# Kernel tuning notes

Hardware: AMD Instinct MI355X
Metric: run time of the kernel (lower is better)

## Reference

```python
import jax, jax.numpy as jnp
import numpy as np

B, T, D, H = 4, 2048, 1024, 16
HD = D // H  # head dim = 64


def setup_inputs() -> dict:
    key = jax.random.key(0)
    ks = jax.random.split(key, 9)
    s_in = 1.0 / np.sqrt(D)
    return {
        "token_embedding": jax.random.normal(ks[0], (B, T, D), dtype=jnp.float32),
        # per-head projections, batched over head axis: [H, D, HD]
        "Wq": jax.random.normal(ks[1], (H, D, HD), dtype=jnp.float32) * s_in,
        "bq": jnp.zeros((H, HD), dtype=jnp.float32),
        "Wk": jax.random.normal(ks[2], (H, D, HD), dtype=jnp.float32) * s_in,
        "bk": jnp.zeros((H, HD), dtype=jnp.float32),
        "Wv": jax.random.normal(ks[3], (H, D, HD), dtype=jnp.float32) * s_in,
        "bv": jnp.zeros((H, HD), dtype=jnp.float32),
        "Wo": jax.random.normal(ks[4], (D, D), dtype=jnp.float32) * s_in,
        "bo": jnp.zeros((D,), dtype=jnp.float32),
    }


def _mha(x, Wq, bq, Wk, bk, Wv, bv, Wo, bo):
    # x: [B,T,D]; per-head proj -> [B,H,T,HD]
    q = jnp.einsum('btd,hde->bhte', x, Wq) + bq[None, :, None, :]
    k = jnp.einsum('btd,hde->bhte', x, Wk) + bk[None, :, None, :]
    v = jnp.einsum('btd,hde->bhte', x, Wv) + bv[None, :, None, :]
    scores = jnp.einsum('bhte,bhse->bhts', q, k) / jnp.sqrt(jnp.float32(HD))
    causal = jnp.tril(jnp.ones((T, T), dtype=bool))
    scores = jnp.where(causal[None, None], scores, jnp.float32(-jnp.inf))
    attn = jax.nn.softmax(scores, axis=-1)
    ctx = jnp.einsum('bhts,bhse->bhte', attn, v)  # [B,H,T,HD]
    # concat heads (head order matches ModuleList order) -> [B,T,D]
    cat = jnp.transpose(ctx, (0, 2, 1, 3)).reshape(B, T, D)
    return cat @ Wo + bo


def reference(token_embedding, Wq, bq, Wk, bk, Wv, bv, Wo, bo):
    return _mha(token_embedding, Wq, bq, Wk, bk, Wv, bv, Wo, bo)
```

## Files before the change

### kernel.cpp

```cpp
#include <hip/hip_runtime.h>
#include <hip/hip_bf16.h>
#include <stdint.h>
#include <stddef.h>

#define B_ 4
#define T_ 2048
#define D_ 1024
#define H_ 16
#define HD_ 64
#define LDQKV (3 * D_)

typedef __attribute__((ext_vector_type(8))) __bf16 bf16x8;
typedef __attribute__((ext_vector_type(4))) float f32x4;
typedef __attribute__((ext_vector_type(16))) float f32x16;

#define AS1V const __attribute__((address_space(1))) void*
#define AS3V __attribute__((address_space(3))) void*

__device__ inline float cross32_max(float x) { return fmaxf(x, __shfl_xor(x, 32)); }
__device__ inline float cross32_sum(float x) { return x + __shfl_xor(x, 32); }

__global__ void cvt_x_kernel(const float* __restrict__ x, __bf16* __restrict__ xb, int n8) {
    int stride = gridDim.x * blockDim.x;
    for (int i = blockIdx.x * blockDim.x + threadIdx.x; i < n8; i += stride) {
        const float4* p = (const float4*)(x + (size_t)i * 8);
        float4 a = p[0], b = p[1];
        bf16x8 o;
        o[0] = (__bf16)a.x; o[1] = (__bf16)a.y; o[2] = (__bf16)a.z; o[3] = (__bf16)a.w;
        o[4] = (__bf16)b.x; o[5] = (__bf16)b.y; o[6] = (__bf16)b.z; o[7] = (__bf16)b.w;
        *(bf16x8*)(xb + (size_t)i * 8) = o;
    }
}

__global__ void build_wT_kernel(const float* __restrict__ Wq, const float* __restrict__ Wk,
                                const float* __restrict__ Wv, __bf16* __restrict__ wT) {
    int which = blockIdx.x, h = blockIdx.y, d0 = blockIdx.z * 4;
    const float* W = (which == 0) ? Wq : (which == 1) ? Wk : Wv;
    int e = threadIdx.x & 63, dd = threadIdx.x >> 6;
    float v = W[((size_t)h * D_ + d0 + dd) * HD_ + e];
    wT[((size_t)which * D_ + h * HD_ + e) * D_ + d0 + dd] = (__bf16)v;
}

__global__ void build_woT_kernel(const float* __restrict__ Wo, __bf16* __restrict__ woT) {
    int k = blockIdx.x;
    for (int n = threadIdx.x; n < D_; n += blockDim.x)
        woT[(size_t)n * D_ + k] = (__bf16)Wo[(size_t)k * D_ + n];
}

__global__ void build_bias_kernel(const float* __restrict__ bq, const float* __restrict__ bk,
                                  const float* __restrict__ bv, float* __restrict__ bqkv) {
    int n = blockIdx.x * blockDim.x + threadIdx.x;
    if (n >= 3 * D_) return;
    const float* b = (n < D_) ? bq : (n < 2 * D_) ? bk : bv;
    bqkv[n] = b[n & (D_ - 1)];
}

template <typename OutT>
__global__ __launch_bounds__(256, 3)
void gemm_bt_kernel(const __bf16* __restrict__ A, const __bf16* __restrict__ Bt,
                    OutT* __restrict__ C, const float* __restrict__ bias,
                    int M, int N, int K, int lda, int ldb, int ldc) {
    __shared__ __bf16 lsA[128 * 64];
    __shared__ __bf16 lsB[128 * 64];
    const int tid = threadIdx.x;
    const int lane = tid & 63;
    const int wave = tid >> 6;
    const int wr = wave >> 1, wc = wave & 1;
    const int lc = lane & 15, lg = lane >> 4;
    const long row0 = (long)blockIdx.y * 128;
    const long col0 = (long)blockIdx.x * 128;

    f32x4 acc[4][4];
#pragma unroll
    for (int mi = 0; mi < 4; mi++)
#pragma unroll
        for (int ni = 0; ni < 4; ni++)
#pragma unroll
            for (int q = 0; q < 4; q++) acc[mi][ni][q] = 0.f;

    const int s_row = tid >> 3, s_k8 = tid & 7;

    for (int k0 = 0; k0 < K; k0 += 64) {
        __syncthreads();
#pragma unroll
        for (int c2 = 0; c2 < 4; c2++) {
            const __bf16* ga = A + (row0 + c2 * 32 + s_row) * (long)lda + k0 + s_k8 * 8;
            const __bf16* gb = Bt + (col0 + c2 * 32 + s_row) * (long)ldb + k0 + s_k8 * 8;
            __bf16* la = lsA + ((c2 << 8) + (wave << 6)) * 8;
            __bf16* lb = lsB + ((c2 << 8) + (wave << 6)) * 8;
            __builtin_amdgcn_global_load_lds((AS1V)ga, (AS3V)la, 16, 0, 0);
            __builtin_amdgcn_global_load_lds((AS1V)gb, (AS3V)lb, 16, 0, 0);
        }
        __syncthreads();
#pragma unroll
        for (int kk = 0; kk < 2; kk++) {
            bf16x8 af[4], bf_[4];
#pragma unroll
            for (int mi = 0; mi < 4; mi++)
                af[mi] = *(const bf16x8*)(lsA + (wr * 64 + mi * 16 + lc) * 64 + (kk * 4 + lg) * 8);
#pragma unroll
            for (int ni = 0; ni < 4; ni++)
                bf_[ni] = *(const bf16x8*)(lsB + (wc * 64 + ni * 16 + lc) * 64 + (kk * 4 + lg) * 8);
#pragma unroll
            for (int mi = 0; mi < 4; mi++)
#pragma unroll
                for (int ni = 0; ni < 4; ni++)
                    acc[mi][ni] =
                        __builtin_amdgcn_mfma_f32_16x16x32_bf16(af[mi], bf_[ni], acc[mi][ni], 0, 0, 0);
        }
    }

#pragma unroll
    for (int mi = 0; mi < 4; mi++) {
#pragma unroll
        for (int ni = 0; ni < 4; ni++) {
            long r0 = row0 + wr * 64 + mi * 16 + lg * 4;
            long cc = col0 + wc * 64 + ni * 16 + lc;
            float bv = bias[cc];
#pragma unroll
            for (int q = 0; q < 4; q++) {
                float v = acc[mi][ni][q] + bv;
                C[(r0 + q) * (long)ldc + cc] = (OutT)v;
            }
        }
    }
}

__global__ void transpose_v_kernel(const __bf16* __restrict__ qkv, __bf16* __restrict__ vT) {
    __shared__ __bf16 tile[64][72];
    const int bh = blockIdx.y, t0 = blockIdx.x * 64;
    const int b = bh >> 4, h = bh & 15;
    const int r = threadIdx.x >> 2, c16 = (threadIdx.x & 3) * 16;
    const __bf16* src = qkv + (size_t)(b * T_ + t0 + r) * LDQKV + 2 * D_ + h * HD_ + c16;
    *(bf16x8*)&tile[r][c16] = *(const bf16x8*)src;
    *(bf16x8*)&tile[r][c16 + 8] = *(const bf16x8*)(src + 8);
    __syncthreads();
    bf16x8 v0, v1;
#pragma unroll
    for (int j = 0; j < 8; j++) v0[j] = tile[c16 + j][r];
#pragma unroll
    for (int j = 0; j < 8; j++) v1[j] = tile[c16 + 8 + j][r];
    __bf16* dst = vT + (size_t)(bh * HD_ + r) * T_ + t0 + c16;
    *(bf16x8*)dst = v0;
    *(bf16x8*)(dst + 8) = v1;
}

__global__ __launch_bounds__(256, 4)
void attn_kernel(const __bf16* __restrict__ qkv, const __bf16* __restrict__ vT,
                 __bf16* __restrict__ ctx) {
    __shared__ __bf16 lsK[64 * 64];
    __shared__ __bf16 lsV[64 * 64];
    const int tid = threadIdx.x;
    const int lane = tid & 63, w = tid >> 6;
    const int l31 = lane & 31, hi = lane >> 5;
    const int bid = blockIdx.x;
    const int xcd = bid & 7, idx = bid >> 3;
    const int bh = xcd * 8 + (idx & 7);
    const int slot = idx >> 3;
    const int chunk = (int)((0x742065138ADC9BEFULL >> (slot * 4)) & 15ULL);
    const int b = bh >> 4, h = bh & 15;
    const float K2 = 0.125f * 1.44269504f;

    const __bf16* kbase = qkv + (size_t)(b * T_) * LDQKV + D_ + h * HD_;
    const __bf16* vbase = vT + (size_t)bh * HD_ * T_;

    int s_row[2], s_ch[2];
#pragma unroll
    for (int c2 = 0; c2 < 2; c2++) {
        int idx2 = c2 * 256 + tid;
        s_row[c2] = idx2 >> 3;
        s_ch[c2] = idx2 & 7;
    }

    const int q0 = chunk * 128;
    const int qw = q0 + w * 32;
    const int myq = qw + l31;

    const __bf16* qbase = qkv + (size_t)(b * T_ + myq) * LDQKV + h * HD_;
    bf16x8 qf[4];
#pragma unroll
    for (int kf = 0; kf < 4; kf++) qf[kf] = *(const bf16x8*)(qbase + kf * 16 + hi * 8);

    f32x16 accO[2];
#pragma unroll
    for (int eo = 0; eo < 2; eo++)
#pragma unroll
        for (int r = 0; r < 16; r++) accO[eo][r] = 0.f;
    float m_r = -1e30f, l_r = 0.f;

    bf16x8 rK[2], rV[2];
    auto loadKV = [&](int kv0) {
#pragma unroll
        for (int c2 = 0; c2 < 2; c2++) {
            rK[c2] = *(const bf16x8*)(kbase + (size_t)(kv0 + s_row[c2]) * LDQKV + s_ch[c2] * 8);
            rV[c2] = *(const bf16x8*)(vbase + (size_t)s_row[c2] * T_ + kv0 + s_ch[c2] * 8);
        }
    };

    const int ntiles = 2 * (chunk + 1);
    loadKV(0);
    for (int it = 0; it < ntiles; ++it) {
        const int kv0 = it << 6;
        __syncthreads();
#pragma unroll
        for (int c2 = 0; c2 < 2; c2++) {
            *(bf16x8*)(lsK + s_row[c2] * 64 + ((s_ch[c2] ^ (s_row[c2] & 7)) << 3)) = rK[c2];
            *(bf16x8*)(lsV + s_row[c2] * 64 + ((s_ch[c2] ^ (s_row[c2] & 7)) << 3)) = rV[c2];
        }
        __syncthreads();
        if (it + 1 < ntiles) loadKV((it + 1) << 6);

        if (kv0 > qw + 31) continue;

        f32x16 st[2];
        __builtin_amdgcn_s_setprio(1);
#pragma unroll
        for (int kh = 0; kh < 2; kh++) {
            f32x16 a;
#pragma unroll
            for (int r = 0; r < 16; r++) a[r] = 0.f;
#pragma unroll
            for (int kf = 0; kf < 4; kf++) {
                int row = kh * 32 + l31;
                int ch = (kf << 1) | hi;
                bf16x8 kfrag = *(const bf16x8*)(lsK + row * 64 + ((ch ^ (row & 7)) << 3));
                a = __builtin_amdgcn_mfma_f32_32x32x16_bf16(kfrag, qf[kf], a, 0, 0, 0);
            }
            st[kh] = a;
        }
        __builtin_amdgcn_s_setprio(0);

        if (kv0 + 63 > qw) {
            const int qmk = myq - kv0 - 4 * hi;
#pragma unroll
            for (int kh = 0; kh < 2; kh++)
#pragma unroll
                for (int r = 0; r < 16; r++) {
                    int kvl = (r & 3) + 8 * (r >> 2) + kh * 32;
                    if (kvl > qmk) st[kh][r] = -1e30f;
                }
        }

        float red[16];
#pragma unroll
        for (int r = 0; r < 16; r++) red[r] = fmaxf(st[0][r], st[1][r]);
#pragma unroll
        for (int s2 = 8; s2 >= 1; s2 >>= 1)
#pragma unroll
            for (int r = 0; r < s2; r++) red[r] = fmaxf(red[r], red[r + s2]);
        float pmax = cross32_max(red[0]);

        if (!__all(pmax - m_r <= 64.f)) {
            float m_new = fmaxf(m_r, pmax);
            float alpha = exp2f((m_r - m_new) * K2);
            l_r *= alpha;
#pragma unroll
            for (int eo = 0; eo < 2; eo++)
#pragma unroll
                for (int r = 0; r < 16; r++) accO[eo][r] *= alpha;
            m_r = m_new;
        }

        const float mb = m_r * K2;
#pragma unroll
        for (int kh = 0; kh < 2; kh++)
#pragma unroll
            for (int r = 0; r < 16; r++) st[kh][r] = exp2f(fmaf(st[kh][r], K2, -mb));

        float sr[16];
#pragma unroll
        for (int r = 0; r < 16; r++) sr[r] = st[0][r] + st[1][r];
#pragma unroll
        for (int s2 = 8; s2 >= 1; s2 >>= 1)
#pragma unroll
            for (int r = 0; r < s2; r++) sr[r] += sr[r + s2];
        l_r += cross32_sum(sr[0]);

        union BW { unsigned u[4]; bf16x8 v; };
        bf16x8 pfrag[4];
        auto pack2 = [](float a, float b) -> unsigned {
            union { __bf16 h[2]; unsigned u; } x;
            x.h[0] = (__bf16)a;
            x.h[1] = (__bf16)b;
            return x.u;
        };
#pragma unroll
        for (int kh = 0; kh < 2; kh++)
#pragma unroll
            for (int sub = 0; sub < 2; sub++) {
                int base = sub * 8;
                unsigned W1 = pack2(st[kh][base + 0], st[kh][base + 1]);
                unsigned W3 = pack2(st[kh][base + 2], st[kh][base + 3]);
                unsigned W2 = pack2(st[kh][base + 4], st[kh][base + 5]);
                unsigned W4 = pack2(st[kh][base + 6], st[kh][base + 7]);
                unsigned X1 = (unsigned)__shfl_xor((int)W1, 32);
                unsigned X2 = (unsigned)__shfl_xor((int)W2, 32);
                unsigned X3 = (unsigned)__shfl_xor((int)W3, 32);
                unsigned X4 = (unsigned)__shfl_xor((int)W4, 32);
                BW bw;
                bw.u[0] = hi ? X2 : W1;
                bw.u[1] = hi ? X4 : W3;
                bw.u[2] = hi ? W2 : X1;
                bw.u[3] = hi ? W4 : X3;
                pfrag[kh * 2 + sub] = bw.v;
            }

        __builtin_amdgcn_s_setprio(1);
#pragma unroll
        for (int eo = 0; eo < 2; eo++) {
#pragma unroll
            for (int ks = 0; ks < 4; ks++) {
                int row = eo * 32 + l31;
                int ch = (ks << 1) | hi;
                bf16x8 vfrag = *(const bf16x8*)(lsV + row * 64 + ((ch ^ (row & 7)) << 3));
                accO[eo] = __builtin_amdgcn_mfma_f32_32x32x16_bf16(vfrag, pfrag[ks], accO[eo], 0, 0, 0);
            }
        }
        __builtin_amdgcn_s_setprio(0);
    }

    float invl = 1.0f / l_r;
    __bf16* cb = ctx + (size_t)(b * T_ + myq) * D_ + h * HD_;
#pragma unroll
    for (int eo = 0; eo < 2; eo++)
#pragma unroll
        for (int r = 0; r < 16; r++) {
            int e = eo * 32 + (r & 3) + 8 * (r >> 2) + 4 * hi;
            cb[e] = (__bf16)(accO[eo][r] * invl);
        }
}

extern "C" void kernel_launch(void* const* d_in, const int* in_sizes, int n_in,
                              void* d_out, int out_size, void* d_ws, size_t ws_size,
                              hipStream_t stream) {
    const float* x = (const float*)d_in[0];
    const float* Wq = (const float*)d_in[1];
    const float* bq = (const float*)d_in[2];
    const float* Wk = (const float*)d_in[3];
    const float* bk = (const float*)d_in[4];
    const float* Wv = (const float*)d_in[5];
    const float* bv = (const float*)d_in[6];
    const float* Wo = (const float*)d_in[7];
    const float* bo = (const float*)d_in[8];
    float* out = (float*)d_out;

    char* ws = (char*)d_ws;
    size_t off = 0;
    auto alloc = [&](size_t bytes) -> void* {
        off = (off + 255) & ~(size_t)255;
        void* p = ws + off;
        off += bytes;
        return p;
    };
    __bf16* xb = (__bf16*)alloc((size_t)B_ * T_ * D_ * 2);
    __bf16* wT = (__bf16*)alloc((size_t)3 * D_ * D_ * 2);
    float* bqkv = (float*)alloc((size_t)3 * D_ * 4);
    __bf16* woT = (__bf16*)alloc((size_t)D_ * D_ * 2);
    __bf16* qkv = (__bf16*)alloc((size_t)B_ * T_ * 3 * D_ * 2);
    __bf16* vTb = (__bf16*)alloc((size_t)B_ * H_ * HD_ * T_ * 2);
    __bf16* ctx = (__bf16*)alloc((size_t)B_ * T_ * D_ * 2);
    (void)ws_size;
    (void)in_sizes;
    (void)n_in;
    (void)out_size;

    cvt_x_kernel<<<2048, 256, 0, stream>>>(x, xb, B_ * T_ * D_ / 8);
    build_wT_kernel<<<dim3(3, H_, D_ / 4), 256, 0, stream>>>(Wq, Wk, Wv, wT);
    build_woT_kernel<<<D_, 256, 0, stream>>>(Wo, woT);
    build_bias_kernel<<<12, 256, 0, stream>>>(bq, bk, bv, bqkv);

    gemm_bt_kernel<__bf16><<<dim3(3 * D_ / 128, B_ * T_ / 128), 256, 0, stream>>>(
        xb, wT, qkv, bqkv, B_ * T_, 3 * D_, D_, D_, D_, 3 * D_);

    transpose_v_kernel<<<dim3(T_ / 64, B_ * H_), 256, 0, stream>>>(qkv, vTb);

    attn_kernel<<<1024, 256, 0, stream>>>(qkv, vTb, ctx);

    gemm_bt_kernel<float><<<dim3(D_ / 128, B_ * T_ / 128), 256, 0, stream>>>(
        ctx, woT, out, bo, B_ * T_, D_, D_, D_, D_, D_);
}
```

Before: 228.8 us.

## Double-buffer 128-wide KV tiles in LDS for causal attention kernel

The attention kernel now stages 128-row K/V tiles into double-buffered LDS. This drops to one barrier per tile and lets the next tile's global loads run while the current tile is computed in two 64-wide sub-steps. The block-to-chunk mapping is replaced by a simple descending/ascending order, and the GEMM launch-bounds occupancy hint is raised from 3 to 4. LDS use grows fourfold, so attention occupancy drops (launch bounds lowered to 2) and register pressure rises from the extra prefetch registers.

```diff
diff --git a/kernel.cpp b/kernel.cpp
--- a/kernel.cpp
+++ b/kernel.cpp
@@ -56,7 +56,7 @@
 }
 
 template <typename OutT>
-__global__ __launch_bounds__(256, 3)
+__global__ __launch_bounds__(256, 4)
 void gemm_bt_kernel(const __bf16* __restrict__ A, const __bf16* __restrict__ Bt,
                     OutT* __restrict__ C, const float* __restrict__ bias,
                     int M, int N, int K, int lda, int ldb, int ldc) {
@@ -145,11 +145,11 @@
     *(bf16x8*)(dst + 8) = v1;
 }
 
-__global__ __launch_bounds__(256, 4)
+__global__ __launch_bounds__(256, 2)
 void attn_kernel(const __bf16* __restrict__ qkv, const __bf16* __restrict__ vT,
                  __bf16* __restrict__ ctx) {
-    __shared__ __bf16 lsK[64 * 64];
-    __shared__ __bf16 lsV[64 * 64];
+    __shared__ __bf16 lsK[2][128 * 64];
+    __shared__ __bf16 lsV[2][64 * 128];
     const int tid = threadIdx.x;
     const int lane = tid & 63, w = tid >> 6;
     const int l31 = lane & 31, hi = lane >> 5;
@@ -157,19 +157,19 @@
     const int xcd = bid & 7, idx = bid >> 3;
     const int bh = xcd * 8 + (idx & 7);
     const int slot = idx >> 3;
-    const int chunk = (int)((0x742065138ADC9BEFULL >> (slot * 4)) & 15ULL);
+    const int chunk = (slot < 8) ? (15 - slot) : (slot - 8);
     const int b = bh >> 4, h = bh & 15;
     const float K2 = 0.125f * 1.44269504f;
 
     const __bf16* kbase = qkv + (size_t)(b * T_) * LDQKV + D_ + h * HD_;
     const __bf16* vbase = vT + (size_t)bh * HD_ * T_;
 
-    int s_row[2], s_ch[2];
-#pragma unroll
-    for (int c2 = 0; c2 < 2; c2++) {
-        int idx2 = c2 * 256 + tid;
-        s_row[c2] = idx2 >> 3;
-        s_ch[c2] = idx2 & 7;
+    int krow[4], kch[4], vrow[4], vch[4];
+#pragma unroll
+    for (int c = 0; c < 4; c++) {
+        int i2 = c * 256 + tid;
+        krow[c] = i2 >> 3;  kch[c] = i2 & 7;
+        vrow[c] = i2 >> 4;  vch[c] = i2 & 15;
     }
 
     const int q0 = chunk * 128;
@@ -188,135 +188,152 @@
         for (int r = 0; r < 16; r++) accO[eo][r] = 0.f;
     float m_r = -1e30f, l_r = 0.f;
 
-    bf16x8 rK[2], rV[2];
+    bf16x8 rK[4], rV[4];
     auto loadKV = [&](int kv0) {
 #pragma unroll
-        for (int c2 = 0; c2 < 2; c2++) {
-            rK[c2] = *(const bf16x8*)(kbase + (size_t)(kv0 + s_row[c2]) * LDQKV + s_ch[c2] * 8);
-            rV[c2] = *(const bf16x8*)(vbase + (size_t)s_row[c2] * T_ + kv0 + s_ch[c2] * 8);
+        for (int c = 0; c < 4; c++) {
+            rK[c] = *(const bf16x8*)(kbase + (size_t)(kv0 + krow[c]) * LDQKV + kch[c] * 8);
+            rV[c] = *(const bf16x8*)(vbase + (size_t)vrow[c] * T_ + kv0 + vch[c] * 8);
         }
     };
-
-    const int ntiles = 2 * (chunk + 1);
+    auto writeLDS = [&](int bi) {
+#pragma unroll
+        for (int c = 0; c < 4; c++) {
+            *(bf16x8*)(&lsK[bi][0] + krow[c] * 64 + ((kch[c] ^ (krow[c] & 7)) << 3)) = rK[c];
+            *(bf16x8*)(&lsV[bi][0] + vrow[c] * 128 + ((vch[c] ^ (vrow[c] & 15)) << 3)) = rV[c];
+        }
+    };
+
+    const int ntiles = chunk + 1;
     loadKV(0);
+    writeLDS(0);
+    if (ntiles > 1) loadKV(128);
+    __syncthreads();
+    int cur = 0;
+
     for (int it = 0; it < ntiles; ++it) {
-        const int kv0 = it << 6;
-        __syncthreads();
-#pragma unroll
-        for (int c2 = 0; c2 < 2; c2++) {
-            *(bf16x8*)(lsK + s_row[c2] * 64 + ((s_ch[c2] ^ (s_row[c2] & 7)) << 3)) = rK[c2];
-            *(bf16x8*)(lsV + s_row[c2] * 64 + ((s_ch[c2] ^ (s_row[c2] & 7)) << 3)) = rV[c2];
-        }
-        __syncthreads();
-        if (it + 1 < ntiles) loadKV((it + 1) << 6);
-
-        if (kv0 > qw + 31) continue;
-
-        f32x16 st[2];
-        __builtin_amdgcn_s_setprio(1);
-#pragma unroll
-        for (int kh = 0; kh < 2; kh++) {
-            f32x16 a;
-#pragma unroll
-            for (int r = 0; r < 16; r++) a[r] = 0.f;
-#pragma unroll
-            for (int kf = 0; kf < 4; kf++) {
-                int row = kh * 32 + l31;
-                int ch = (kf << 1) | hi;
-                bf16x8 kfrag = *(const bf16x8*)(lsK + row * 64 + ((ch ^ (row & 7)) << 3));
-                a = __builtin_amdgcn_mfma_f32_32x32x16_bf16(kfrag, qf[kf], a, 0, 0, 0);
-            }
-            st[kh] = a;
-        }
-        __builtin_amdgcn_s_setprio(0);
-
-        if (kv0 + 63 > qw) {
-            const int qmk = myq - kv0 - 4 * hi;
+        const int kv0 = it << 7;
+        const __bf16* lk = &lsK[cur][0];
+        const __bf16* lv = &lsV[cur][0];
+
+#pragma unroll
+        for (int sub = 0; sub < 2; ++sub) {
+            const int kv0s = kv0 + sub * 64;
+            if (kv0s > qw + 31) break;
+
+            f32x16 st[2];
+            __builtin_amdgcn_s_setprio(1);
+#pragma unroll
+            for (int kh = 0; kh < 2; kh++) {
+                f32x16 a;
+#pragma unroll
+                for (int r = 0; r < 16; r++) a[r] = 0.f;
+#pragma unroll
+                for (int kf = 0; kf < 4; kf++) {
+                    int row = sub * 64 + kh * 32 + l31;
+                    int ch = (kf << 1) | hi;
+                    bf16x8 kfrag = *(const bf16x8*)(lk + row * 64 + ((ch ^ (row & 7)) << 3));
+                    a = __builtin_amdgcn_mfma_f32_32x32x16_bf16(kfrag, qf[kf], a, 0, 0, 0);
+                }
+                st[kh] = a;
+            }
+            __builtin_amdgcn_s_setprio(0);
+
+            if (kv0s + 63 > qw) {
+                const int qmk = myq - kv0s - 4 * hi;
+#pragma unroll
+                for (int kh = 0; kh < 2; kh++)
+#pragma unroll
+                    for (int r = 0; r < 16; r++) {
+                        int kvl = (r & 3) + 8 * (r >> 2) + kh * 32;
+                        if (kvl > qmk) st[kh][r] = -1e30f;
+                    }
+            }
+
+            float red[16];
+#pragma unroll
+            for (int r = 0; r < 16; r++) red[r] = fmaxf(st[0][r], st[1][r]);
+#pragma unroll
+            for (int s2 = 8; s2 >= 1; s2 >>= 1)
+#pragma unroll
+                for (int r = 0; r < s2; r++) red[r] = fmaxf(red[r], red[r + s2]);
+            float pmax = cross32_max(red[0]);
+
+            if (!__all(pmax - m_r <= 64.f)) {
+                float m_new = fmaxf(m_r, pmax);
+                float alpha = exp2f((m_r - m_new) * K2);
+                l_r *= alpha;
+#pragma unroll
+                for (int eo = 0; eo < 2; eo++)
+#pragma unroll
+                    for (int r = 0; r < 16; r++) accO[eo][r] *= alpha;
+                m_r = m_new;
+            }
+
+            const float mb = m_r * K2;
 #pragma unroll
             for (int kh = 0; kh < 2; kh++)
 #pragma unroll
-                for (int r = 0; r < 16; r++) {
-                    int kvl = (r & 3) + 8 * (r >> 2) + kh * 32;
-                    if (kvl > qmk) st[kh][r] = -1e30f;
+                for (int r = 0; r < 16; r++) st[kh][r] = exp2f(fmaf(st[kh][r], K2, -mb));
+
+            float sr[16];
+#pragma unroll
+            for (int r = 0; r < 16; r++) sr[r] = st[0][r] + st[1][r];
+#pragma unroll
+            for (int s2 = 8; s2 >= 1; s2 >>= 1)
+#pragma unroll
+                for (int r = 0; r < s2; r++) sr[r] += sr[r + s2];
+            l_r += cross32_sum(sr[0]);
+
+            union BW { unsigned u[4]; bf16x8 v; };
+            bf16x8 pfrag[4];
+            auto pack2 = [](float a, float b) -> unsigned {
+                union { __bf16 h[2]; unsigned u; } x;
+                x.h[0] = (__bf16)a;
+                x.h[1] = (__bf16)b;
+                return x.u;
+            };
+#pragma unroll
+            for (int kh = 0; kh < 2; kh++)
+#pragma unroll
+                for (int sb = 0; sb < 2; sb++) {
+                    int base = sb * 8;
+                    unsigned W1 = pack2(st[kh][base + 0], st[kh][base + 1]);
+                    unsigned W3 = pack2(st[kh][base + 2], st[kh][base + 3]);
+                    unsigned W2 = pack2(st[kh][base + 4], st[kh][base + 5]);
+                    unsigned W4 = pack2(st[kh][base + 6], st[kh][base + 7]);
+                    unsigned X1 = (unsigned)__shfl_xor((int)W1, 32);
+                    unsigned X2 = (unsigned)__shfl_xor((int)W2, 32);
+                    unsigned X3 = (unsigned)__shfl_xor((int)W3, 32);
+                    unsigned X4 = (unsigned)__shfl_xor((int)W4, 32);
+                    BW bw;
+                    bw.u[0] = hi ? X2 : W1;
+                    bw.u[1] = hi ? X4 : W3;
+                    bw.u[2] = hi ? W2 : X1;
+                    bw.u[3] = hi ? W4 : X3;
+                    pfrag[kh * 2 + sb] = bw.v;
                 }
-        }
-
-        float red[16];
-#pragma unroll
-        for (int r = 0; r < 16; r++) red[r] = fmaxf(st[0][r], st[1][r]);
-#pragma unroll
-        for (int s2 = 8; s2 >= 1; s2 >>= 1)
-#pragma unroll
-            for (int r = 0; r < s2; r++) red[r] = fmaxf(red[r], red[r + s2]);
-        float pmax = cross32_max(red[0]);
-
-        if (!__all(pmax - m_r <= 64.f)) {
-            float m_new = fmaxf(m_r, pmax);
-            float alpha = exp2f((m_r - m_new) * K2);
-            l_r *= alpha;
-#pragma unroll
-            for (int eo = 0; eo < 2; eo++)
-#pragma unroll
-                for (int r = 0; r < 16; r++) accO[eo][r] *= alpha;
-            m_r = m_new;
-        }
-
-        const float mb = m_r * K2;
-#pragma unroll
-        for (int kh = 0; kh < 2; kh++)
-#pragma unroll
-            for (int r = 0; r < 16; r++) st[kh][r] = exp2f(fmaf(st[kh][r], K2, -mb));
-
-        float sr[16];
-#pragma unroll
-        for (int r = 0; r < 16; r++) sr[r] = st[0][r] + st[1][r];
-#pragma unroll
-        for (int s2 = 8; s2 >= 1; s2 >>= 1)
-#pragma unroll
-            for (int r = 0; r < s2; r++) sr[r] += sr[r + s2];
-        l_r += cross32_sum(sr[0]);
-
-        union BW { unsigned u[4]; bf16x8 v; };
-        bf16x8 pfrag[4];
-        auto pack2 = [](float a, float b) -> unsigned {
-            union { __bf16 h[2]; unsigned u; } x;
-            x.h[0] = (__bf16)a;
-            x.h[1] = (__bf16)b;
-            return x.u;
-        };
-#pragma unroll
-        for (int kh = 0; kh < 2; kh++)
-#pragma unroll
-            for (int sub = 0; sub < 2; sub++) {
-                int base = sub * 8;
-                unsigned W1 = pack2(st[kh][base + 0], st[kh][base + 1]);
-                unsigned W3 = pack2(st[kh][base + 2], st[kh][base + 3]);
-                unsigned W2 = pack2(st[kh][base + 4], st[kh][base + 5]);
-                unsigned W4 = pack2(st[kh][base + 6], st[kh][base + 7]);
-                unsigned X1 = (unsigned)__shfl_xor((int)W1, 32);
-                unsigned X2 = (unsigned)__shfl_xor((int)W2, 32);
-                unsigned X3 = (unsigned)__shfl_xor((int)W3, 32);
-                unsigned X4 = (unsigned)__shfl_xor((int)W4, 32);
-                BW bw;
-                bw.u[0] = hi ? X2 : W1;
-                bw.u[1] = hi ? X4 : W3;
-                bw.u[2] = hi ? W2 : X1;
-                bw.u[3] = hi ? W4 : X3;
-                pfrag[kh * 2 + sub] = bw.v;
-            }
-
-        __builtin_amdgcn_s_setprio(1);
-#pragma unroll
-        for (int eo = 0; eo < 2; eo++) {
-#pragma unroll
-            for (int ks = 0; ks < 4; ks++) {
-                int row = eo * 32 + l31;
-                int ch = (ks << 1) | hi;
-                bf16x8 vfrag = *(const bf16x8*)(lsV + row * 64 + ((ch ^ (row & 7)) << 3));
-                accO[eo] = __builtin_amdgcn_mfma_f32_32x32x16_bf16(vfrag, pfrag[ks], accO[eo], 0, 0, 0);
-            }
-        }
-        __builtin_amdgcn_s_setprio(0);
+
+            __builtin_amdgcn_s_setprio(1);
+#pragma unroll
+            for (int eo = 0; eo < 2; eo++) {
+#pragma unroll
+                for (int ks = 0; ks < 4; ks++) {
+                    int row = eo * 32 + l31;
+                    int cc = sub * 8 + ((ks << 1) | hi);
+                    bf16x8 vfrag = *(const bf16x8*)(lv + row * 128 + ((cc ^ (row & 15)) << 3));
+                    accO[eo] = __builtin_amdgcn_mfma_f32_32x32x16_bf16(vfrag, pfrag[ks], accO[eo], 0, 0, 0);
+                }
+            }
+            __builtin_amdgcn_s_setprio(0);
+        }
+
+        if (it + 1 < ntiles) {
+            writeLDS(cur ^ 1);
+            if (it + 2 < ntiles) loadKV((it + 2) << 7);
+            __syncthreads();
+            cur ^= 1;
+        }
     }
 
     float invl = 1.0f / l_r;
```

Result: no change. 231.2 us (+1.1%).
